# Kernel tuning notes

Measured on AMD Instinct MI355X. Metric: run time of the kernel, lower is better.

Reference implementation:

```python
import jax, jax.numpy as jnp
import numpy as np

GAMMA = 2.0
EPS = 1e-6

B, C = 4096, 32000


def setup_inputs() -> dict:
    key = jax.random.key(0)
    k1, k2 = jax.random.split(key)
    pred = jax.random.normal(k1, (B, C), dtype=jnp.float32)
    target = jax.random.randint(k2, (B,), 0, C, dtype=jnp.int64)
    return {"pred": pred, "target": target}


def reference(pred, target):
    # pred: [B, C] logits, target: [B] int class labels
    b, c = pred.shape
    beta = (b - 1) / b
    logp = jax.nn.log_softmax(pred, axis=1)                      # [B, C]
    # Faithful to original: entropy_b = target_b * sum_c (1-p)^gamma * logp
    # (the torch code multiplies by the scalar class index b_target)
    focal = jnp.sum(jnp.power(1.0 - jnp.exp(logp), GAMMA) * logp, axis=1)  # [B]
    ent = target.astype(pred.dtype) * focal                     # [B]
    # class-balanced aggregation: bucket per class label
    counts = jax.ops.segment_sum(jnp.ones((b,), pred.dtype), target, num_segments=c)  # n_c
    cls_sum = jax.ops.segment_sum(ent, target, num_segments=c)  # sum of entropies per class
    w = (1.0 - beta) / (1.0 - jnp.power(jnp.asarray(beta, pred.dtype), counts) + EPS)
    # classes absent from batch have cls_sum == 0 exactly, so they contribute 0
    return (-1.0 / b) * jnp.sum(w * cls_sum)
```

## Files before the change

kernel.cpp:

```cpp
#include <hip/hip_runtime.h>
#include <math.h>

#define NROWS 4096
#define NCLS  32000
#define VEC_PER_ROW (NCLS / 4)
#define BLK 1024
#define EPSF 1e-6f

#define LNBETA (-2.4417042724800387e-4f)
#define WNUM 2.44140625e-4f

__device__ __forceinline__ float max4(float4 v) {
    return fmaxf(fmaxf(v.x, v.y), fmaxf(v.z, v.w));
}
__device__ __forceinline__ float sum4(float4 v) {
    return (v.x + v.y) + (v.z + v.w);
}

__global__ __launch_bounds__(BLK) void focal_kernel(const float* __restrict__ pred,
                                                    float* __restrict__ focal_out)
{
    const int row = blockIdx.x;
    const int tid = threadIdx.x;
    const float4* rp = reinterpret_cast<const float4*>(pred) + (size_t)row * VEC_PER_ROW;

    float4 x[8];
#pragma unroll
    for (int i = 0; i < 7; ++i) x[i] = rp[tid + i * BLK];
    const bool lv = (tid + 7 * BLK) < VEC_PER_ROW;
    if (lv) x[7] = rp[tid + 7 * BLK];
    else    x[7] = make_float4(-1e30f, -1e30f, -1e30f, -1e30f);

    float m = -1e30f, s1 = 0.0f;
#pragma unroll
    for (int i = 0; i < 7; ++i) { m = fmaxf(m, max4(x[i])); s1 += sum4(x[i]); }
    m = fmaxf(m, max4(x[7]));
    if (lv) s1 += sum4(x[7]);

    __shared__ float sm[16], ss[16];
#pragma unroll
    for (int off = 32; off > 0; off >>= 1) {
        m  = fmaxf(m, __shfl_xor(m, off));
        s1 += __shfl_xor(s1, off);
    }
    const int wid = tid >> 6;
    const int lane = tid & 63;
    if (lane == 0) { sm[wid] = m; ss[wid] = s1; }
    __syncthreads();
    if (tid < 64) {
        float mm = (tid < 16) ? sm[tid] : -1e30f;
        float s  = (tid < 16) ? ss[tid] : 0.0f;
#pragma unroll
        for (int off = 8; off > 0; off >>= 1) {
            mm = fmaxf(mm, __shfl_xor(mm, off));
            s += __shfl_xor(s, off);
        }
        if (tid == 0) { sm[0] = mm; ss[0] = s; }
    }
    __syncthreads();
    const float M  = sm[0];
    const float S1 = ss[0];

    float Z = 0.f, A = 0.f, Z2 = 0.f, A2 = 0.f;
#pragma unroll
    for (int i = 0; i < 8; ++i) {
        float vals[4] = {x[i].x, x[i].y, x[i].z, x[i].w};
#pragma unroll
        for (int j = 0; j < 4; ++j) {
            float t = vals[j] - M;
            float e = exp2f(t * 1.44269504088896340736f);
            Z += e;
            A = fmaf(e, t, A);
            float e2 = e * e;
            Z2 += e2;
            A2 = fmaf(e2, t, A2);
        }
    }

    __shared__ float r0[16], r1[16], r2[16], r3[16];
#pragma unroll
    for (int off = 32; off > 0; off >>= 1) {
        Z  += __shfl_xor(Z,  off);
        A  += __shfl_xor(A,  off);
        Z2 += __shfl_xor(Z2, off);
        A2 += __shfl_xor(A2, off);
    }
    if (lane == 0) { r0[wid] = Z; r1[wid] = A; r2[wid] = Z2; r3[wid] = A2; }
    __syncthreads();
    if (tid < 64) {
        float a = (tid < 16) ? r0[tid] : 0.f;
        float b = (tid < 16) ? r1[tid] : 0.f;
        float c = (tid < 16) ? r2[tid] : 0.f;
        float d = (tid < 16) ? r3[tid] : 0.f;
#pragma unroll
        for (int off = 8; off > 0; off >>= 1) {
            a += __shfl_xor(a, off);
            b += __shfl_xor(b, off);
            c += __shfl_xor(c, off);
            d += __shfl_xor(d, off);
        }
        if (tid == 0) {
            float lnZ  = log2f(a) * 0.69314718055994530942f;
            float invZ = 1.0f / a;
            float T = S1 - (float)NCLS * M;
            float focal = (T - (float)NCLS * lnZ)
                        - 2.0f * (b * invZ - lnZ)
                        + (d - lnZ * c) * (invZ * invZ);
            focal_out[row] = focal;
        }
    }
}

__global__ void count_kernel(const int* __restrict__ target, int* __restrict__ counts)
{
    int b = blockIdx.x * blockDim.x + threadIdx.x;
    if (b < NROWS) atomicAdd(&counts[target[b]], 1);
}

__global__ __launch_bounds__(1024) void finalize_kernel(const int* __restrict__ target,
                                                        const float* __restrict__ focal,
                                                        const int* __restrict__ counts,
                                                        float* __restrict__ out)
{
    const int tid = threadIdx.x;
    double local = 0.0;
    for (int b = tid; b < NROWS; b += 1024) {
        int t = target[b];
        int n = counts[t];
        float u = (float)n * LNBETA;
        float denom;
        if (u > -0.25f) {
            denom = -(u * (1.f + u * (0.5f + u * (0.16666667f + u * 0.041666667f))));
        } else {
            denom = 1.f - __expf(u);
        }
        float w = WNUM / (denom + EPSF);
        local += (double)(w * (float)t * focal[b]);
    }

    __shared__ double rd[16];
#pragma unroll
    for (int off = 32; off > 0; off >>= 1) local += __shfl_xor(local, off);
    const int wid = tid >> 6, lane = tid & 63;
    if (lane == 0) rd[wid] = local;
    __syncthreads();
    if (tid < 64) {
        double v = (tid < 16) ? rd[tid] : 0.0;
#pragma unroll
        for (int off = 8; off > 0; off >>= 1) v += __shfl_xor(v, off);
        if (tid == 0) out[0] = (float)(v * (-1.0 / (double)NROWS));
    }
}

extern "C" void kernel_launch(void* const* d_in, const int* in_sizes, int n_in,
                              void* d_out, int out_size, void* d_ws, size_t ws_size,
                              hipStream_t stream)
{
    const float* pred  = (const float*)d_in[0];
    const int* target  = (const int*)d_in[1];
    float* out         = (float*)d_out;

    float* focal = (float*)d_ws;
    int* counts  = (int*)((char*)d_ws + NROWS * sizeof(float));

    hipMemsetAsync(counts, 0, NCLS * sizeof(int), stream);
    focal_kernel<<<NROWS, BLK, 0, stream>>>(pred, focal);
    count_kernel<<<(NROWS + 255) / 256, 256, 0, stream>>>(target, counts);
    finalize_kernel<<<1, 1024, 0, stream>>>(target, focal, counts, out);
}
```

Before: 107.3 us.

## Fuse class counting into finalize via packed shared-memory histogram; halve focal block size

The memset and the separate count kernel are removed. Class counts are now built inside the single-block finalize kernel as a shared-memory histogram that packs two 16-bit counters per 32-bit word, which removes two launches and a global-memory round trip. The focal kernel also drops from 1024 to 512 threads per block with 16 float4 registers per thread and a launch_bounds occupancy hint, which raises register pressure in exchange for cheaper block-level reductions. The 16-bit packed counters assume that no class occurs more than 65535 times, which holds because there are only 4096 rows.

```diff
diff --git a/kernel.cpp b/kernel.cpp
--- a/kernel.cpp
+++ b/kernel.cpp
@@ -4,7 +4,9 @@
 #define NROWS 4096
 #define NCLS  32000
 #define VEC_PER_ROW (NCLS / 4)
-#define BLK 1024
+#define BLK 512
+#define NV  16
+#define TAIL (VEC_PER_ROW - (NV - 1) * BLK)
 #define EPSF 1e-6f
 
 #define LNBETA (-2.4417042724800387e-4f)
@@ -17,41 +19,41 @@
     return (v.x + v.y) + (v.z + v.w);
 }
 
-__global__ __launch_bounds__(BLK) void focal_kernel(const float* __restrict__ pred,
-                                                    float* __restrict__ focal_out)
+__global__ __launch_bounds__(BLK, 4) void focal_kernel(const float* __restrict__ pred,
+                                                       float* __restrict__ focal_out)
 {
     const int row = blockIdx.x;
     const int tid = threadIdx.x;
     const float4* rp = reinterpret_cast<const float4*>(pred) + (size_t)row * VEC_PER_ROW;
 
-    float4 x[8];
+    float4 x[NV];
 #pragma unroll
-    for (int i = 0; i < 7; ++i) x[i] = rp[tid + i * BLK];
-    const bool lv = (tid + 7 * BLK) < VEC_PER_ROW;
-    if (lv) x[7] = rp[tid + 7 * BLK];
-    else    x[7] = make_float4(-1e30f, -1e30f, -1e30f, -1e30f);
+    for (int i = 0; i < NV - 1; ++i) x[i] = rp[tid + i * BLK];
+    const bool lv = tid < TAIL;
+    if (lv) x[NV - 1] = rp[tid + (NV - 1) * BLK];
+    else    x[NV - 1] = make_float4(-1e30f, -1e30f, -1e30f, -1e30f);
 
     float m = -1e30f, s1 = 0.0f;
 #pragma unroll
-    for (int i = 0; i < 7; ++i) { m = fmaxf(m, max4(x[i])); s1 += sum4(x[i]); }
-    m = fmaxf(m, max4(x[7]));
-    if (lv) s1 += sum4(x[7]);
+    for (int i = 0; i < NV - 1; ++i) { m = fmaxf(m, max4(x[i])); s1 += sum4(x[i]); }
+    m = fmaxf(m, max4(x[NV - 1]));
+    if (lv) s1 += sum4(x[NV - 1]);
 
-    __shared__ float sm[16], ss[16];
+    __shared__ float sm[8], ss[8];
 #pragma unroll
     for (int off = 32; off > 0; off >>= 1) {
         m  = fmaxf(m, __shfl_xor(m, off));
         s1 += __shfl_xor(s1, off);
     }
-    const int wid = tid >> 6;
+    const int wid  = tid >> 6;
     const int lane = tid & 63;
     if (lane == 0) { sm[wid] = m; ss[wid] = s1; }
     __syncthreads();
     if (tid < 64) {
-        float mm = (tid < 16) ? sm[tid] : -1e30f;
-        float s  = (tid < 16) ? ss[tid] : 0.0f;
+        float mm = (tid < 8) ? sm[tid] : -1e30f;
+        float s  = (tid < 8) ? ss[tid] : 0.0f;
 #pragma unroll
-        for (int off = 8; off > 0; off >>= 1) {
+        for (int off = 4; off > 0; off >>= 1) {
             mm = fmaxf(mm, __shfl_xor(mm, off));
             s += __shfl_xor(s, off);
         }
@@ -63,7 +65,7 @@
 
     float Z = 0.f, A = 0.f, Z2 = 0.f, A2 = 0.f;
 #pragma unroll
-    for (int i = 0; i < 8; ++i) {
+    for (int i = 0; i < NV; ++i) {
         float vals[4] = {x[i].x, x[i].y, x[i].z, x[i].w};
 #pragma unroll
         for (int j = 0; j < 4; ++j) {
@@ -77,7 +79,7 @@
         }
     }
 
-    __shared__ float r0[16], r1[16], r2[16], r3[16];
+    __shared__ float r0[8], r1[8], r2[8], r3[8];
 #pragma unroll
     for (int off = 32; off > 0; off >>= 1) {
         Z  += __shfl_xor(Z,  off);
@@ -88,12 +90,12 @@
     if (lane == 0) { r0[wid] = Z; r1[wid] = A; r2[wid] = Z2; r3[wid] = A2; }
     __syncthreads();
     if (tid < 64) {
-        float a = (tid < 16) ? r0[tid] : 0.f;
-        float b = (tid < 16) ? r1[tid] : 0.f;
-        float c = (tid < 16) ? r2[tid] : 0.f;
-        float d = (tid < 16) ? r3[tid] : 0.f;
+        float a = (tid < 8) ? r0[tid] : 0.f;
+        float b = (tid < 8) ? r1[tid] : 0.f;
+        float c = (tid < 8) ? r2[tid] : 0.f;
+        float d = (tid < 8) ? r3[tid] : 0.f;
 #pragma unroll
-        for (int off = 8; off > 0; off >>= 1) {
+        for (int off = 4; off > 0; off >>= 1) {
             a += __shfl_xor(a, off);
             b += __shfl_xor(b, off);
             c += __shfl_xor(c, off);
@@ -111,22 +113,28 @@
     }
 }
 
-__global__ void count_kernel(const int* __restrict__ target, int* __restrict__ counts)
-{
-    int b = blockIdx.x * blockDim.x + threadIdx.x;
-    if (b < NROWS) atomicAdd(&counts[target[b]], 1);
-}
-
 __global__ __launch_bounds__(1024) void finalize_kernel(const int* __restrict__ target,
                                                         const float* __restrict__ focal,
-                                                        const int* __restrict__ counts,
                                                         float* __restrict__ out)
 {
+    __shared__ unsigned int cnt[NCLS / 2];
+    __shared__ double rd[16];
     const int tid = threadIdx.x;
+
+    uint4* c4 = reinterpret_cast<uint4*>(cnt);
+    for (int i = tid; i < NCLS / 8; i += 1024) c4[i] = make_uint4(0u, 0u, 0u, 0u);
+    __syncthreads();
+
+    for (int b = tid; b < NROWS; b += 1024) {
+        int t = target[b];
+        atomicAdd(&cnt[t >> 1], 1u << ((t & 1) * 16));
+    }
+    __syncthreads();
+
     double local = 0.0;
     for (int b = tid; b < NROWS; b += 1024) {
         int t = target[b];
-        int n = counts[t];
+        int n = (int)((cnt[t >> 1] >> ((t & 1) * 16)) & 0xffffu);
         float u = (float)n * LNBETA;
         float denom;
         if (u > -0.25f) {
@@ -138,7 +146,6 @@
         local += (double)(w * (float)t * focal[b]);
     }
 
-    __shared__ double rd[16];
 #pragma unroll
     for (int off = 32; off > 0; off >>= 1) local += __shfl_xor(local, off);
     const int wid = tid >> 6, lane = tid & 63;
@@ -161,10 +168,7 @@
     float* out         = (float*)d_out;
 
     float* focal = (float*)d_ws;
-    int* counts  = (int*)((char*)d_ws + NROWS * sizeof(float));
 
-    hipMemsetAsync(counts, 0, NCLS * sizeof(int), stream);
     focal_kernel<<<NROWS, BLK, 0, stream>>>(pred, focal);
-    count_kernel<<<(NROWS + 255) / 256, 256, 0, stream>>>(target, counts);
-    finalize_kernel<<<1, 1024, 0, stream>>>(target, focal, counts, out);
+    finalize_kernel<<<1, 1024, 0, stream>>>(target, focal, out);
 }
```

Measured after the change: 99.61 us (median of 2 runs). -7.2%, faster.
